# Performance work log

Hardware: AMD Instinct MI355X
Metric: run time of the kernel (lower is better)

Reference implementation:

```python
import jax, jax.numpy as jnp
from jax import lax
import numpy as np

R = 3                 # corr_radius (args.small)
NUM_LEVELS = 4        # corr_levels
SCALES = (8, 8, 4, 4, 2, 2)


def conv2d(x, w, b, pad):
    y = lax.conv_general_dilated(x, w, (1, 1), [(pad, pad), (pad, pad)],
                                 dimension_numbers=('NCHW', 'OIHW', 'NCHW'))
    return y + b[None, :, None, None]


def avg_pool2(x):
    return lax.reduce_window(x, 0.0, lax.add, (1, 1, 2, 2), (1, 1, 2, 2), 'VALID') * 0.25


def coords_grid(b, h, w):
    y, x = jnp.meshgrid(jnp.arange(h, dtype=jnp.float32), jnp.arange(w, dtype=jnp.float32), indexing='ij')
    return jnp.broadcast_to(jnp.stack([x, y])[None], (b, 2, h, w))


def bilinear_sample(img, coords):
    # img [N,C,H,W]; coords [N,Hg,Wg,2] (x,y) pixel coords; zeros padding, align_corners=True
    N, C, H, W = img.shape
    Hg, Wg = coords.shape[1], coords.shape[2]
    x, y = coords[..., 0], coords[..., 1]
    x0 = jnp.floor(x)
    y0 = jnp.floor(y)
    wx = x - x0
    wy = y - y0
    flat = img.reshape(N, C, H * W)

    def gather(xi, yi):
        valid = (xi >= 0) & (xi <= W - 1) & (yi >= 0) & (yi <= H - 1)
        xi_c = jnp.clip(xi, 0, W - 1).astype(jnp.int32)
        yi_c = jnp.clip(yi, 0, H - 1).astype(jnp.int32)
        idx = (yi_c * W + xi_c).reshape(N, 1, Hg * Wg)
        v = jnp.take_along_axis(flat, jnp.broadcast_to(idx, (N, C, Hg * Wg)), axis=2)
        return v * valid.reshape(N, 1, Hg * Wg)

    w00 = ((1 - wx) * (1 - wy)).reshape(N, 1, -1)
    w10 = (wx * (1 - wy)).reshape(N, 1, -1)
    w01 = ((1 - wx) * wy).reshape(N, 1, -1)
    w11 = (wx * wy).reshape(N, 1, -1)
    out = (gather(x0, y0) * w00 + gather(x0 + 1, y0) * w10
           + gather(x0, y0 + 1) * w01 + gather(x0 + 1, y0 + 1) * w11)
    return out.reshape(N, C, Hg, Wg)


def corr_pyramid(f1, f2):
    B, C, H, W = f1.shape
    corr = jnp.einsum('bchw,bcuv->bhwuv', f1, f2) / jnp.sqrt(jnp.float32(C))
    corr = corr.reshape(B * H * W, 1, H, W)
    pyr = [corr]
    for _ in range(NUM_LEVELS - 1):
        corr = avg_pool2(corr)
        pyr.append(corr)
    return pyr


def corr_lookup(pyr, coords):
    B, _, H, W = coords.shape
    c = coords.transpose(0, 2, 3, 1).reshape(B * H * W, 1, 1, 2)
    d = jnp.arange(-R, R + 1, dtype=jnp.float32)
    dy, dx = jnp.meshgrid(d, d, indexing='ij')
    # upstream RAFT adds stack(meshgrid(dy,dx)) to (x,y); window is symmetric so keep its ordering
    delta = jnp.stack([dy, dx], axis=-1)[None]  # [1,2R+1,2R+1,2]
    outs = []
    for i, corr in enumerate(pyr):
        cl = c / (2.0 ** i) + delta
        sampled = bilinear_sample(corr, cl)  # [B*H*W,1,2R+1,2R+1]
        outs.append(sampled.reshape(B, H, W, -1))
    return jnp.concatenate(outs, axis=-1).transpose(0, 3, 1, 2)


def interp_mat(n_in, n_out):
    # bilinear, align_corners=True
    pos = jnp.linspace(0.0, n_in - 1.0, n_out)
    i0 = jnp.clip(jnp.floor(pos).astype(jnp.int32), 0, n_in - 2)
    w = pos - i0
    M = jnp.zeros((n_out, n_in), jnp.float32)
    M = M.at[jnp.arange(n_out), i0].add(1.0 - w)
    M = M.at[jnp.arange(n_out), i0 + 1].add(w)
    return M


def upflow_n(flow, n):
    B, C, H, W = flow.shape
    My = interp_mat(H, n * H)
    Mx = interp_mat(W, n * W)
    return n * jnp.einsum('ph,bchw,qw->bcpq', My, flow, Mx)


def small_update(net, inp, corr, flow, p):
    # SmallMotionEncoder
    cor = jax.nn.relu(conv2d(corr, p['convc1_w'], p['convc1_b'], 0))
    flo = jax.nn.relu(conv2d(flow, p['convf1_w'], p['convf1_b'], 3))
    flo = jax.nn.relu(conv2d(flo, p['convf2_w'], p['convf2_b'], 1))
    mot = jax.nn.relu(conv2d(jnp.concatenate([cor, flo], 1), p['convm_w'], p['convm_b'], 1))
    x = jnp.concatenate([inp, mot, flow], 1)  # 64 + 80 + 2 = 146 ch
    # ConvGRU
    hx = jnp.concatenate([net, x], 1)
    z = jax.nn.sigmoid(conv2d(hx, p['convz_w'], p['convz_b'], 1))
    r = jax.nn.sigmoid(conv2d(hx, p['convr_w'], p['convr_b'], 1))
    q = jnp.tanh(conv2d(jnp.concatenate([r * net, x], 1), p['convq_w'], p['convq_b'], 1))
    net = (1.0 - z) * net + z * q
    # FlowHead
    df = conv2d(jax.nn.relu(conv2d(net, p['fh1_w'], p['fh1_b'], 1)), p['fh2_w'], p['fh2_b'], 1)
    return net, df


def raft_forward(fmap1_2, fmap2_2, fmap1_4, fmap2_4, fmap1_8, fmap2_8,
                 net2, inp2, net4, inp4, net8, inp8,
                 convc1_w, convc1_b, convf1_w, convf1_b, convf2_w, convf2_b,
                 convm_w, convm_b, convz_w, convz_b, convr_w, convr_b,
                 convq_w, convq_b, fh1_w, fh1_b, fh2_w, fh2_b):
    p = dict(convc1_w=convc1_w, convc1_b=convc1_b, convf1_w=convf1_w, convf1_b=convf1_b,
             convf2_w=convf2_w, convf2_b=convf2_b, convm_w=convm_w, convm_b=convm_b,
             convz_w=convz_w, convz_b=convz_b, convr_w=convr_w, convr_b=convr_b,
             convq_w=convq_w, convq_b=convq_b, fh1_w=fh1_w, fh1_b=fh1_b, fh2_w=fh2_w, fh2_b=fh2_b)
    fmaps = {2: (fmap1_2, fmap2_2), 4: (fmap1_4, fmap2_4), 8: (fmap1_8, fmap2_8)}
    pyr = {s: corr_pyramid(*fmaps[s]) for s in (2, 4, 8)}
    net = {2: jnp.tanh(net2), 4: jnp.tanh(net4), 8: jnp.tanh(net8)}
    inp = {2: jax.nn.relu(inp2), 4: jax.nn.relu(inp4), 8: jax.nn.relu(inp8)}
    B = fmap1_8.shape[0]
    coords0 = {s: coords_grid(B, fmaps[s][0].shape[2], fmaps[s][0].shape[3]) for s in (2, 4, 8)}
    coords1 = {s: coords0[s] for s in (2, 4, 8)}
    preds = []
    for s in SCALES:
        c1 = lax.stop_gradient(coords1[s])  # .detach()
        corr = corr_lookup(pyr[s], c1)
        flow = c1 - coords0[s]
        net[s], df = small_update(net[s], inp[s], corr, flow, p)
        coords1[s] = c1 + df
        preds.append(upflow_n(coords1[s] - coords0[s], s))
        if s > 2:
            coords1[s // 2] = upflow_n(coords1[s], 2)
    return jnp.stack(preds)  # [6, B, 2, 192, 192]


def setup_inputs():
    key = jax.random.key(0)
    specs = {
        'fmap1_2': (1, 128, 96, 96), 'fmap2_2': (1, 128, 96, 96),
        'fmap1_4': (1, 128, 48, 48), 'fmap2_4': (1, 128, 48, 48),
        'fmap1_8': (1, 128, 24, 24), 'fmap2_8': (1, 128, 24, 24),
        'net2': (1, 96, 96, 96), 'inp2': (1, 64, 96, 96),
        'net4': (1, 96, 48, 48), 'inp4': (1, 64, 48, 48),
        'net8': (1, 96, 24, 24), 'inp8': (1, 64, 24, 24),
        'convc1_w': (96, 196, 1, 1), 'convc1_b': (96,),
        'convf1_w': (64, 2, 7, 7), 'convf1_b': (64,),
        'convf2_w': (32, 64, 3, 3), 'convf2_b': (32,),
        'convm_w': (80, 128, 3, 3), 'convm_b': (80,),
        'convz_w': (96, 242, 3, 3), 'convz_b': (96,),
        'convr_w': (96, 242, 3, 3), 'convr_b': (96,),
        'convq_w': (96, 242, 3, 3), 'convq_b': (96,),
        'fh1_w': (128, 96, 3, 3), 'fh1_b': (128,),
        'fh2_w': (2, 128, 3, 3), 'fh2_b': (2,),
    }
    out = {}
    for i, (name, shp) in enumerate(specs.items()):
        scale = 0.1 if ('_w' in name or '_b' in name) else 1.0
        out[name] = jax.random.normal(jax.random.fold_in(key, i), shp, dtype=jnp.float32) * scale
    return out


def reference(fmap1_2, fmap2_2, fmap1_4, fmap2_4, fmap1_8, fmap2_8,
              net2, inp2, net4, inp4, net8, inp8,
              convc1_w, convc1_b, convf1_w, convf1_b, convf2_w, convf2_b,
              convm_w, convm_b, convz_w, convz_b, convr_w, convr_b,
              convq_w, convq_b, fh1_w, fh1_b, fh2_w, fh2_b):
    return raft_forward(fmap1_2, fmap2_2, fmap1_4, fmap2_4, fmap1_8, fmap2_8,
                        net2, inp2, net4, inp4, net8, inp8,
                        convc1_w, convc1_b, convf1_w, convf1_b, convf2_w, convf2_b,
                        convm_w, convm_b, convz_w, convz_b, convr_w, convr_b,
                        convq_w, convq_b, fh1_w, fh1_b, fh2_w, fh2_b)
```

## Files before the change

### kernel.cpp

```cpp
#include <hip/hip_runtime.h>
#include <hip/hip_bf16.h>
#include <math.h>


typedef __attribute__((ext_vector_type(8))) short short8;
typedef __attribute__((ext_vector_type(4))) float f32x4;

static inline int nblk(int n, int b){ return (n + b - 1) / b; }

__device__ __forceinline__ short bf16bits(float v){
  __hip_bfloat16 h = __float2bfloat16(v);
  return *reinterpret_cast<short*>(&h);
}
__device__ __forceinline__ float bf2f(short s){
  unsigned u = ((unsigned)(unsigned short)s) << 16;
  return *reinterpret_cast<float*>(&u);
}
__device__ __forceinline__ void split1(float v, unsigned short* hi, unsigned short* lo){
  short h = bf16bits(v);
  *hi = (unsigned short)h;
  *lo = (unsigned short)bf16bits(v - bf2f(h));
}
__device__ __forceinline__ int xcd_swz(int bid, int n){
  int q = n >> 3, r = n & 7;
  int x = bid & 7, k = bid >> 3;
  return (x < r ? x*(q+1) : r*(q+1) + (x-r)*q) + k;
}

__global__ void k_init_scale(const float* __restrict__ net_in, const float* __restrict__ inp_in,
                             float* __restrict__ netP, unsigned short* __restrict__ netS,
                             unsigned short* __restrict__ hxS,
                             float* __restrict__ coords, int H, int W)
{
  int HW = H*W;
  int i = blockIdx.x*256 + threadIdx.x;
  if (i >= HW*176) return;
  int p = i / 176, c = i - p*176;
  if (c < 96){
    float t = tanhf(net_in[(size_t)c*HW + p]);
    netP[(size_t)p*96 + c] = t;
    split1(t, &netS[(size_t)p*192 + c], &netS[(size_t)p*192 + 96 + c]);
  } else if (c < 160){
    float r = fmaxf(inp_in[(size_t)(c-96)*HW + p], 0.f);
    split1(r, &hxS[(size_t)p*512 + c], &hxS[(size_t)p*512 + 256 + c]);
  } else if (c < 174){
    int col = 242 + (c - 160);
    hxS[(size_t)p*512 + col] = 0;
    hxS[(size_t)p*512 + 256 + col] = 0;
  } else if (c == 174){
    coords[p] = (float)(p % W);
  } else {
    coords[HW + p] = (float)(p / W);
  }
}
__global__ void k_transpose2(const float* __restrict__ f2, const float* __restrict__ f1,
                             float* __restrict__ f2c, float* __restrict__ f1h, int HW)
{
  int i = blockIdx.x*256 + threadIdx.x;
  int n = HW*128;
  if (i >= 2*n) return;
  if (i < n){
    int p = i >> 7, c = i & 127;
    f2c[((size_t)(c >> 2)*HW + p)*4 + (c & 3)] = f2[c*HW + p];
  } else {
    int k = i - n; int p = k >> 7, c = k & 127;
    f1h[k] = f1[c*HW + p];
  }
}
__global__ void k_pool_c4(const float* __restrict__ in, float* __restrict__ out, int H2, int W2){
  int i = blockIdx.x*256 + threadIdx.x;
  int HW2 = H2*W2;
  int n = 32*HW2*4;
  if (i >= n) return;
  int e = i & 3, rest = i >> 2;
  int p = rest % HW2, cc = rest / HW2;
  int ox = p % W2, oy = p / W2;
  int Win = 2*W2;
  size_t HWin = (size_t)(2*H2)*Win;
  const float* b = in + (cc*HWin + (size_t)(2*oy)*Win + 2*ox)*4 + e;
  out[i] = 0.25f*(b[0] + b[4] + b[(size_t)Win*4] + b[(size_t)Win*4 + 4]);
}
__global__ void k_cat2(const float* __restrict__ a, const float* __restrict__ b,
                       float* __restrict__ o, int n){
  int i = blockIdx.x*256 + threadIdx.x;
  if (i < 2*n) o[i] = (i < n) ? a[i] : b[i-n];
}

__global__ __launch_bounds__(256)
void k_corr4(const float* __restrict__ f1h,
             const float* __restrict__ l0, const float* __restrict__ l1,
             const float* __restrict__ l2, const float* __restrict__ l3,
             const float* __restrict__ coords,
             unsigned short* __restrict__ corrS,
             unsigned short* __restrict__ hxS,
             const unsigned short* __restrict__ netS,
             int H, int W)
{
  int HW = H*W;
  int wv = threadIdx.x >> 6, lane = threadIdx.x & 63;
  int q = blockIdx.x*4 + wv;
  __shared__ __align__(16) float sf1[4][128];
  sf1[wv][lane]      = f1h[(size_t)q*128 + lane];
  sf1[wv][64 + lane] = f1h[(size_t)q*128 + 64 + lane];
  __syncthreads();
  float x = coords[q], y = coords[HW + q];
  const float* const lv[4] = {l0, l1, l2, l3};
  int u = lane & 7, v = lane >> 3;
  int t = lane;
  int j = min(t / 7, 6), k = min(t % 7, 6);
  const float4* a = (const float4*)&sf1[wv][0];
  #pragma unroll
  for (int i = 0; i < 4; i++){
    int Wi = W >> i, Hi = H >> i;
    size_t HWi = (size_t)Wi*Hi;
    float sc = 1.0f / (float)(1 << i);
    float xs = x*sc, ys = y*sc;
    float fx = floorf(xs), fy = floorf(ys);
    float wx = xs - fx, wy = ys - fy;
    float xf = fx + (float)(u - 3);
    float yf = fy + (float)(v - 3);
    float d = 0.0f;
    if (xf >= 0.0f && xf <= (float)(Wi-1) && yf >= 0.0f && yf <= (float)(Hi-1)){
      const float4* b = (const float4*)lv[i] + ((size_t)((int)yf)*Wi + (int)xf);
      float a0 = 0.f, a1 = 0.f, a2 = 0.f, a3 = 0.f;
      #pragma unroll
      for (int kk = 0; kk < 32; kk += 4){
        float4 av0 = a[kk],   bv0 = b[(size_t)kk*HWi];
        float4 av1 = a[kk+1], bv1 = b[(size_t)(kk+1)*HWi];
        float4 av2 = a[kk+2], bv2 = b[(size_t)(kk+2)*HWi];
        float4 av3 = a[kk+3], bv3 = b[(size_t)(kk+3)*HWi];
        a0 = fmaf(av0.x,bv0.x, fmaf(av0.y,bv0.y, fmaf(av0.z,bv0.z, fmaf(av0.w,bv0.w, a0))));
        a1 = fmaf(av1.x,bv1.x, fmaf(av1.y,bv1.y, fmaf(av1.z,bv1.z, fmaf(av1.w,bv1.w, a1))));
        a2 = fmaf(av2.x,bv2.x, fmaf(av2.y,bv2.y, fmaf(av2.z,bv2.z, fmaf(av2.w,bv2.w, a2))));
        a3 = fmaf(av3.x,bv3.x, fmaf(av3.y,bv3.y, fmaf(av3.z,bv3.z, fmaf(av3.w,bv3.w, a3))));
      }
      d = (a0 + a1) + (a2 + a3);
    }
    float d00 = __shfl(d,  k   *8 + j);
    float d10 = __shfl(d,  k   *8 + j + 1);
    float d01 = __shfl(d, (k+1)*8 + j);
    float d11 = __shfl(d, (k+1)*8 + j + 1);
    if (t < 49){
      float val = ((1.f-wx)*(1.f-wy)*d00 + wx*(1.f-wy)*d10
                + (1.f-wx)*wy*d01 + wx*wy*d11) * 0.08838834764831845f;
      split1(val, &corrS[(size_t)q*448 + i*49 + t], &corrS[(size_t)q*448 + 224 + i*49 + t]);
    }
  }
  if (lane < 28){
    corrS[(size_t)q*448 + 196 + lane] = 0;
    corrS[(size_t)q*448 + 224 + 196 + lane] = 0;
  }
  hxS[(size_t)q*512 + lane]       = netS[(size_t)q*192 + lane];
  hxS[(size_t)q*512 + 256 + lane] = netS[(size_t)q*192 + 96 + lane];
  if (lane < 32){
    hxS[(size_t)q*512 + 64 + lane]       = netS[(size_t)q*192 + 64 + lane];
    hxS[(size_t)q*512 + 256 + 64 + lane] = netS[(size_t)q*192 + 96 + 64 + lane];
  } else if (lane == 32){
    split1(x - (float)(q % W), &hxS[(size_t)q*512 + 240], &hxS[(size_t)q*512 + 256 + 240]);
  } else if (lane == 33){
    split1(y - (float)(q / W), &hxS[(size_t)q*512 + 241], &hxS[(size_t)q*512 + 256 + 241]);
  }
}

__global__ void k_upflow2(const float* __restrict__ cin, float* __restrict__ pred,
                          int Hin, int Win, float s,
                          float* __restrict__ conext, int Hf)
{
  int idx = blockIdx.x*256 + threadIdx.x;
  const int HWp = 192*192;
  int c, py, px, Hout, Wout;
  float n; int subtract; float* outp; size_t oidx;
  if (idx < 2*HWp){
    c = idx / HWp; int rem = idx - c*HWp; py = rem / 192; px = rem % 192;
    Hout = 192; Wout = 192; n = s; subtract = 1; outp = pred; oidx = idx;
  } else {
    int k2 = idx - 2*HWp;
    int HWf = Hf*Hf;
    if (Hf == 0 || k2 >= 2*HWf) return;
    c = k2 / HWf; int rem = k2 - c*HWf; py = rem / Hf; px = rem % Hf;
    Hout = Hf; Wout = Hf; n = 2.f; subtract = 0; outp = conext; oidx = k2;
  }
  float posy = (float)py * (float)(Hin-1) / (float)(Hout-1);
  float posx = (float)px * (float)(Win-1) / (float)(Wout-1);
  int iy = (int)floorf(posy); iy = max(0, min(iy, Hin-2));
  int ix = (int)floorf(posx); ix = max(0, min(ix, Win-2));
  float wy = posy - (float)iy, wx = posx - (float)ix;
  const float* base = cin + (size_t)c*Hin*Win;
  float s00 = 0.f, s10 = 0.f, s01 = 0.f, s11 = 0.f;
  if (subtract){
    if (c == 0){ s00 = (float)ix; s01 = (float)ix; s10 = (float)(ix+1); s11 = (float)(ix+1); }
    else       { s00 = (float)iy; s10 = (float)iy; s01 = (float)(iy+1); s11 = (float)(iy+1); }
  }
  float v00 = base[(size_t)iy*Win + ix]       - s00;
  float v10 = base[(size_t)iy*Win + ix + 1]   - s10;
  float v01 = base[(size_t)(iy+1)*Win + ix]   - s01;
  float v11 = base[(size_t)(iy+1)*Win + ix+1] - s11;
  float val = (1.f-wy)*((1.f-wx)*v00 + wx*v10) + wy*((1.f-wx)*v01 + wx*v11);
  outp[oidx] = n * val;
}

__global__ void k_packb(const float* __restrict__ w0, const float* __restrict__ w1,
                        int split, int Cout, int Cin, int KT, int CH32, int mode,
                        short8* __restrict__ out, int nt16, int KTN)
{
  int gid = blockIdx.x*256 + threadIdx.x;
  if (gid >= KTN*nt16*64) return;
  int lane = gid & 63, blk = gid >> 6;
  int ct = blk % nt16, kt = blk / nt16;
  int col = ct*16 + (lane & 15);
  int tap = kt / CH32, chunk = kt - tap*CH32;
  int ci0 = chunk*32 + (lane >> 4)*8;
  short8 hi8, lo8;
  #pragma unroll
  for (int e = 0; e < 8; e++){
    int ci = ci0 + e;
    float v = 0.f;
    if (col < Cout && ci < Cin && tap < KT){
      if (mode == 1){
        v = w0[((size_t)col*2 + (ci & 1))*49 + (ci >> 1)];
      } else {
        const float* wp = (col < split) ? (w0 + (size_t)col*Cin*KT)
                                        : (w1 + (size_t)(col - split)*Cin*KT);
        v = wp[(size_t)ci*KT + tap];
      }
    }
    short h = bf16bits(v);
    hi8[e] = h;
    lo8[e] = bf16bits(v - bf2f(h));
  }
  out[(size_t)blk*128 + lane]      = hi8;
  out[(size_t)blk*128 + 64 + lane] = lo8;
}

template<int KTW, int CH32, int FM, int ACT, int EPI, int NQ, int NF>
__global__ __launch_bounds__(256)
void k_fgemm(const unsigned short* __restrict__ A, int Cpad,
             const float* __restrict__ zr_, const float* __restrict__ net_,
             const float* __restrict__ coF,
             const short8* __restrict__ B, int nt16, const float* __restrict__ bias,
             float* __restrict__ outF, int osF, int ooF,
             unsigned short* __restrict__ outS, int CpadS, int ooS,
             int Cout, int H, int W,
             const float* __restrict__ ez, int ezs,
             const float* __restrict__ eold, int eos)
{
  constexpr int KT = KTW*KTW, P = KTW/2;
  int HW = H*W;
  int lane = threadIdx.x & 63;
  int nb = gridDim.x*gridDim.y;
  int wg = xcd_swz(blockIdx.y*gridDim.x + blockIdx.x, nb);
  int by = wg % gridDim.y;
  int bx = wg / gridDim.y;
  int mt = bx*4 + (threadIdx.x >> 6);
  int ct0 = by*NF;
  int p = mt*16 + (lane & 15);
  int x = p % W, y = p / W;
  int kq = (lane >> 4)*8;

  f32x4 acc[NF];
  #pragma unroll
  for (int f = 0; f < NF; f++) acc[f] = f32x4{0.f,0.f,0.f,0.f};
  const short8 zero8 = short8{0,0,0,0,0,0,0,0};

  #pragma unroll
  for (int tap = 0; tap < KT; tap++){
    const int dx = tap % KTW - P, dy = tap / KTW - P;
    int xx = x + dx, yy = y + dy;
    bool ok = ((unsigned)xx < (unsigned)W) && ((unsigned)yy < (unsigned)H);
    int base = yy*W + xx;
    const unsigned short* arow = A + (size_t)base*2*Cpad;
    #pragma unroll
    for (int c = 0; c < CH32; c++){
      int kt = tap*CH32 + c;
      short8 ah = zero8, al = zero8;
      if constexpr (FM == 2){
        float vv[8];
        #pragma unroll
        for (int e = 0; e < 8; e++){
          int ci = c*32 + kq + e;
          float v = 0.f;
          if (ci < 98){
            int t7 = ci >> 1, jj = ci & 1;
            int ddx = t7 % 7 - 3, ddy = t7 / 7 - 3;
            int x2 = x + ddx, y2 = y + ddy;
            if ((unsigned)x2 < (unsigned)W && (unsigned)y2 < (unsigned)H)
              v = coF[(size_t)jj*HW + y2*W + x2] - (float)(jj ? y2 : x2);
          }
          vv[e] = v;
        }
        #pragma unroll
        for (int e = 0; e < 8; e++){
          short h = bf16bits(vv[e]);
          ah[e] = h;
          al[e] = bf16bits(vv[e] - bf2f(h));
        }
      } else if (NQ > 0 && c < NQ){
        if (ok){
          const float4* zp = (const float4*)(zr_ + (size_t)base*192 + 96 + c*32 + kq);
          const float4* np = (const float4*)(net_ + (size_t)base*96 + c*32 + kq);
          float4 z0 = zp[0], z1 = zp[1], n0 = np[0], n1 = np[1];
          float vv[8] = {z0.x*n0.x, z0.y*n0.y, z0.z*n0.z, z0.w*n0.w,
                         z1.x*n1.x, z1.y*n1.y, z1.z*n1.z, z1.w*n1.w};
          #pragma unroll
          for (int e = 0; e < 8; e++){
            short h = bf16bits(vv[e]);
            ah[e] = h;
            al[e] = bf16bits(vv[e] - bf2f(h));
          }
        }
      } else {
        if (ok){
          const unsigned short* ap = arow + c*32 + kq;
          ah = *(const short8*)ap;
          al = *(const short8*)(ap + Cpad);
        }
      }
      const short8* bp = B + ((size_t)kt*nt16 + ct0)*128 + lane;
      #pragma unroll
      for (int f = 0; f < NF; f++){
        short8 bh = bp[(size_t)f*128], bl = bp[(size_t)f*128 + 64];
        acc[f] = __builtin_amdgcn_mfma_f32_16x16x32_bf16(ah, bh, acc[f], 0, 0, 0);
        acc[f] = __builtin_amdgcn_mfma_f32_16x16x32_bf16(al, bh, acc[f], 0, 0, 0);
        acc[f] = __builtin_amdgcn_mfma_f32_16x16x32_bf16(ah, bl, acc[f], 0, 0, 0);
      }
    }
  }

  int rowb = mt*16 + ((lane >> 4) << 2);
  int colq = lane & 15;
  #pragma unroll
  for (int f = 0; f < NF; f++){
    int col = (ct0 + f)*16 + colq;
    if (col < Cout){
      float bb = bias[col];
      #pragma unroll
      for (int r = 0; r < 4; r++){
        float val = acc[f][r] + bb;
        if (ACT == 1) val = fmaxf(val, 0.f);
        if (ACT == 2) val = 1.f/(1.f + expf(-val));
        if (ACT == 3) val = tanhf(val);
        int row = rowb + r;
        if constexpr (EPI == 2){
          outF[(size_t)col*HW + row] += val;
        } else {
          if constexpr (EPI == 1){
            float zz = ez[(size_t)row*ezs + col];
            val = (1.f - zz)*eold[(size_t)row*eos + col] + zz*val;
          }
          if constexpr (EPI == 1 || EPI == 3)
            outF[(size_t)row*osF + ooF + col] = val;
          if constexpr (EPI == 0 || EPI == 1)
            split1(val, &outS[(size_t)row*2*CpadS + ooS + col],
                        &outS[(size_t)row*2*CpadS + CpadS + ooS + col]);
        }
      }
    }
  }
}

extern "C" void kernel_launch(void* const* d_in, const int* in_sizes, int n_in,
                              void* d_out, int out_size, void* d_ws, size_t ws_size,
                              hipStream_t stream)
{
  (void)in_sizes; (void)n_in; (void)out_size; (void)ws_size;
  const float* f1s[3]    = {(const float*)d_in[0], (const float*)d_in[2], (const float*)d_in[4]};
  const float* f2s[3]    = {(const float*)d_in[1], (const float*)d_in[3], (const float*)d_in[5]};
  const float* net_in[3] = {(const float*)d_in[6], (const float*)d_in[8], (const float*)d_in[10]};
  const float* inp_in[3] = {(const float*)d_in[7], (const float*)d_in[9], (const float*)d_in[11]};
  const float* Wc1 = (const float*)d_in[12]; const float* bc1 = (const float*)d_in[13];
  const float* Wf1 = (const float*)d_in[14]; const float* bf1 = (const float*)d_in[15];
  const float* Wf2 = (const float*)d_in[16]; const float* bf2 = (const float*)d_in[17];
  const float* Wm  = (const float*)d_in[18]; const float* bm  = (const float*)d_in[19];
  const float* Wz  = (const float*)d_in[20]; const float* bz  = (const float*)d_in[21];
  const float* Wr  = (const float*)d_in[22]; const float* br  = (const float*)d_in[23];
  const float* Wq  = (const float*)d_in[24]; const float* bq  = (const float*)d_in[25];
  const float* Wh1 = (const float*)d_in[26]; const float* bh1 = (const float*)d_in[27];
  const float* Wh2 = (const float*)d_in[28]; const float* bh2 = (const float*)d_in[29];

  const int Hs[3] = {96, 48, 24};

  float* ws = (float*)d_ws;
  size_t off = 0;
  auto alloc = [&](size_t nfl)->float*{
    float* p = ws + off;
    off += (nfl + 3) & ~((size_t)3);
    return p;
  };

  float* f2l[3][4]; float* f1h[3]; float* netP[3][2]; float* coords[3];
  unsigned short* netS[3][2]; unsigned short* hxS[3];
  for (int si = 0; si < 3; si++){
    int H = Hs[si], HW = H*H;
    for (int l = 0; l < 4; l++) f2l[si][l] = alloc((size_t)(HW >> (2*l))*128);
    f1h[si]     = alloc((size_t)HW*128);
    netP[si][0] = alloc((size_t)HW*96);
    netP[si][1] = alloc((size_t)HW*96);
    netS[si][0] = (unsigned short*)alloc((size_t)HW*96);
    netS[si][1] = (unsigned short*)alloc((size_t)HW*96);
    hxS[si]     = (unsigned short*)alloc((size_t)HW*256);
    coords[si]  = alloc((size_t)2*HW);
  }
  const int HWm = 96*96;
  unsigned short* corrS = (unsigned short*)alloc((size_t)HWm*224);
  unsigned short* flo1S = (unsigned short*)alloc((size_t)HWm*64);
  unsigned short* cminS = (unsigned short*)alloc((size_t)HWm*128);
  unsigned short* t128S = (unsigned short*)alloc((size_t)HWm*128);
  float* zrb = alloc((size_t)HWm*192);
  float* Bc1 = alloc((size_t)7*6*512);
  float* Bf1 = alloc((size_t)4*4*512);
  float* Bf2 = alloc((size_t)18*2*512);
  float* Bm  = alloc((size_t)36*6*512);
  float* Bzr = alloc((size_t)72*12*512);
  float* Bq  = alloc((size_t)72*6*512);
  float* Bh1 = alloc((size_t)27*8*512);
  float* Bh2 = alloc((size_t)36*1*512);
  float* bzr = alloc(192);

  #define NB(n) dim3((unsigned)nblk((n), 256))

  k_packb<<<NB(7*6*64),  256,0,stream>>>(Wc1, Wc1, 96, 96, 196, 1, 7, 0, (short8*)Bc1, 6, 7);
  k_packb<<<NB(4*4*64),  256,0,stream>>>(Wf1, Wf1, 64, 64,  98, 1, 4, 1, (short8*)Bf1, 4, 4);
  k_packb<<<NB(18*2*64), 256,0,stream>>>(Wf2, Wf2, 32, 32,  64, 9, 2, 0, (short8*)Bf2, 2, 18);
  k_packb<<<NB(36*6*64), 256,0,stream>>>(Wm,  Wm,  80, 80, 128, 9, 4, 0, (short8*)Bm,  6, 36);
  k_packb<<<NB(72*12*64),256,0,stream>>>(Wz,  Wr,  96, 192,242, 9, 8, 0, (short8*)Bzr, 12, 72);
  k_packb<<<NB(72*6*64), 256,0,stream>>>(Wq,  Wq,  96, 96, 242, 9, 8, 0, (short8*)Bq,  6, 72);
  k_packb<<<NB(27*8*64), 256,0,stream>>>(Wh1, Wh1,128, 128, 96, 9, 3, 0, (short8*)Bh1, 8, 27);
  k_packb<<<NB(36*1*64), 256,0,stream>>>(Wh2, Wh2,  2,   2,128, 9, 4, 0, (short8*)Bh2, 1, 36);
  k_cat2<<<dim3(1), 256, 0, stream>>>(bz, br, bzr, 96);

  for (int si = 0; si < 3; si++){
    int H = Hs[si], HW = H*H;
    k_init_scale<<<NB(HW*176), 256,0,stream>>>(net_in[si], inp_in[si], netP[si][0],
                                               netS[si][0], hxS[si], coords[si], H, H);
    k_transpose2<<<NB(2*HW*128), 256,0,stream>>>(f2s[si], f1s[si], f2l[si][0], f1h[si], HW);
    for (int l = 1; l < 4; l++){
      int Hl = H >> l;
      k_pool_c4<<<NB(32*Hl*Hl*4), 256,0,stream>>>(f2l[si][l-1], f2l[si][l], Hl, Hl);
    }
  }

  int cur[3] = {0, 0, 0};
  const int seq[6] = {2, 2, 1, 1, 0, 0};
  for (int it = 0; it < 6; it++){
    int si = seq[it];
    int H = Hs[si], W = H, HW = H*W;
    int MT = HW/16;
    float s = (si == 0) ? 2.0f : ((si == 1) ? 4.0f : 8.0f);
    float* netcF = netP[si][cur[si]];
    float* netnF = netP[si][cur[si]^1];
    unsigned short* netcS = netS[si][cur[si]];
    unsigned short* netnS = netS[si][cur[si]^1];
    float* co = coords[si];
    unsigned short* hx = hxS[si];
    unsigned gx = (unsigned)(MT/4);

    k_corr4<<<dim3((unsigned)(HW/4)), 256,0,stream>>>(
        f1h[si], f2l[si][0], f2l[si][1], f2l[si][2], f2l[si][3], co,
        corrS, hx, netcS, H, W);

    k_fgemm<1,7,0,1,0,0,2><<<dim3(gx,3), 256,0,stream>>>(corrS,224, nullptr,nullptr,nullptr,
        (short8*)Bc1, 6, bc1, nullptr,0,0, cminS,128,0, 96, H,W, nullptr,0, nullptr,0);
    k_fgemm<1,4,2,1,0,0,2><<<dim3(gx,2), 256,0,stream>>>(nullptr,0, nullptr,nullptr,co,
        (short8*)Bf1, 4, bf1, nullptr,0,0, flo1S,64,0, 64, H,W, nullptr,0, nullptr,0);
    k_fgemm<3,2,0,1,0,0,2><<<dim3(gx,1), 256,0,stream>>>(flo1S,64, nullptr,nullptr,nullptr,
        (short8*)Bf2, 2, bf2, nullptr,0,0, cminS,128,96, 32, H,W, nullptr,0, nullptr,0);
    k_fgemm<3,4,0,1,0,0,2><<<dim3(gx,3), 256,0,stream>>>(cminS,128, nullptr,nullptr,nullptr,
        (short8*)Bm, 6, bm, nullptr,0,0, hx,256,160, 80, H,W, nullptr,0, nullptr,0);
    k_fgemm<3,8,0,2,3,0,2><<<dim3(gx,6), 256,0,stream>>>(hx,256, nullptr,nullptr,nullptr,
        (short8*)Bzr, 12, bzr, zrb,192,0, nullptr,0,0, 192, H,W, nullptr,0, nullptr,0);
    k_fgemm<3,8,0,3,1,3,2><<<dim3(gx,3), 256,0,stream>>>(hx,256, zrb,netcF,nullptr,
        (short8*)Bq, 6, bq, netnF,96,0, netnS,96,0, 96, H,W, zrb,192, netcF,96);
    k_fgemm<3,3,0,1,0,0,2><<<dim3(gx,4), 256,0,stream>>>(netnS,96, nullptr,nullptr,nullptr,
        (short8*)Bh1, 8, bh1, nullptr,0,0, t128S,128,0, 128, H,W, nullptr,0, nullptr,0);
    k_fgemm<3,4,0,0,2,0,1><<<dim3(gx,1), 256,0,stream>>>(t128S,128, nullptr,nullptr,nullptr,
        (short8*)Bh2, 1, bh2, co,0,0, nullptr,0,0, 2, H,W, nullptr,0, nullptr,0);

    int Hf = (si > 0) ? Hs[si-1] : 0;
    float* conext = (si > 0) ? coords[si-1] : nullptr;
    k_upflow2<<<NB(2*192*192 + (Hf ? 2*Hf*Hf : 0)), 256,0,stream>>>(
        co, (float*)d_out + (size_t)it*2*192*192, H, W, s, conext, Hf);

    cur[si] ^= 1;
  }
  #undef NB
}
```

Measured before the change: 1.335 ms.

## Store bf16 activations in zero-padded halo layout and widen N-tiles for largest scale

Intermediate split-bf16 activation buffers (net, hx, flow, corr-motion, hidden) are now allocated per scale with a one-pixel zero border and memset once, so the 3x3 conv GEMM loads no longer need bounds checks or predicated zero fills. Epilogues write into the padded coordinates. For the largest scale, the GEMMs also use more output fragments per wave (NF 3 or 4) with fewer column blocks, trading more registers for better B-operand reuse and fewer A reloads. Costs are extra memory, a memset, and per-scale buffer copies instead of shared ones.

Result: slower. 1.454 ms (+8.9%).

```diff
diff --git a/kernel.cpp b/kernel.cpp
--- a/kernel.cpp
+++ b/kernel.cpp
@@ -34,20 +34,18 @@
 {
   int HW = H*W;
   int i = blockIdx.x*256 + threadIdx.x;
-  if (i >= HW*176) return;
-  int p = i / 176, c = i - p*176;
+  if (i >= HW*162) return;
+  int p = i / 162, c = i - p*162;
+  int PW = W + 2;
+  size_t pq = (size_t)(p / W + 1)*PW + (p % W) + 1;
   if (c < 96){
     float t = tanhf(net_in[(size_t)c*HW + p]);
     netP[(size_t)p*96 + c] = t;
-    split1(t, &netS[(size_t)p*192 + c], &netS[(size_t)p*192 + 96 + c]);
+    split1(t, &netS[pq*192 + c], &netS[pq*192 + 96 + c]);
   } else if (c < 160){
     float r = fmaxf(inp_in[(size_t)(c-96)*HW + p], 0.f);
-    split1(r, &hxS[(size_t)p*512 + c], &hxS[(size_t)p*512 + 256 + c]);
-  } else if (c < 174){
-    int col = 242 + (c - 160);
-    hxS[(size_t)p*512 + col] = 0;
-    hxS[(size_t)p*512 + 256 + col] = 0;
-  } else if (c == 174){
+    split1(r, &hxS[pq*512 + c], &hxS[pq*512 + 256 + c]);
+  } else if (c == 160){
     coords[p] = (float)(p % W);
   } else {
     coords[HW + p] = (float)(p / W);
@@ -150,15 +148,17 @@
     corrS[(size_t)q*448 + 196 + lane] = 0;
     corrS[(size_t)q*448 + 224 + 196 + lane] = 0;
   }
-  hxS[(size_t)q*512 + lane]       = netS[(size_t)q*192 + lane];
-  hxS[(size_t)q*512 + 256 + lane] = netS[(size_t)q*192 + 96 + lane];
+  int PW = W + 2;
+  size_t pq = (size_t)(q / W + 1)*PW + (q % W) + 1;
+  hxS[pq*512 + lane]       = netS[pq*192 + lane];
+  hxS[pq*512 + 256 + lane] = netS[pq*192 + 96 + lane];
   if (lane < 32){
-    hxS[(size_t)q*512 + 64 + lane]       = netS[(size_t)q*192 + 64 + lane];
-    hxS[(size_t)q*512 + 256 + 64 + lane] = netS[(size_t)q*192 + 96 + 64 + lane];
+    hxS[pq*512 + 64 + lane]       = netS[pq*192 + 64 + lane];
+    hxS[pq*512 + 256 + 64 + lane] = netS[pq*192 + 96 + 64 + lane];
   } else if (lane == 32){
-    split1(x - (float)(q % W), &hxS[(size_t)q*512 + 240], &hxS[(size_t)q*512 + 256 + 240]);
+    split1(x - (float)(q % W), &hxS[pq*512 + 240], &hxS[pq*512 + 256 + 240]);
   } else if (lane == 33){
-    split1(y - (float)(q / W), &hxS[(size_t)q*512 + 241], &hxS[(size_t)q*512 + 256 + 241]);
+    split1(y - (float)(q / W), &hxS[pq*512 + 241], &hxS[pq*512 + 256 + 241]);
   }
 }
 
@@ -232,7 +232,7 @@
   out[(size_t)blk*128 + 64 + lane] = lo8;
 }
 
-template<int KTW, int CH32, int FM, int ACT, int EPI, int NQ, int NF>
+template<int KTW, int CH32, int FM, int ACT, int EPI, int NQ, int NF, int PAD>
 __global__ __launch_bounds__(256)
 void k_fgemm(const unsigned short* __restrict__ A, int Cpad,
              const float* __restrict__ zr_, const float* __restrict__ net_,
@@ -246,6 +246,7 @@
 {
   constexpr int KT = KTW*KTW, P = KTW/2;
   int HW = H*W;
+  int PW = W + 2;
   int lane = threadIdx.x & 63;
   int nb = gridDim.x*gridDim.y;
   int wg = xcd_swz(blockIdx.y*gridDim.x + blockIdx.x, nb);
@@ -266,9 +267,17 @@
   for (int tap = 0; tap < KT; tap++){
     const int dx = tap % KTW - P, dy = tap / KTW - P;
     int xx = x + dx, yy = y + dy;
-    bool ok = ((unsigned)xx < (unsigned)W) && ((unsigned)yy < (unsigned)H);
-    int base = yy*W + xx;
-    const unsigned short* arow = A + (size_t)base*2*Cpad;
+    const unsigned short* arow;
+    bool ok;
+    if (PAD){
+      arow = A + (size_t)((yy+1)*PW + xx + 1)*2*Cpad;
+      ok = true;
+    } else {
+      ok = ((unsigned)xx < (unsigned)W) && ((unsigned)yy < (unsigned)H);
+      arow = A + (size_t)(yy*W + xx)*2*Cpad;
+    }
+    int baseu = yy*W + xx;
+    bool okq = ((unsigned)xx < (unsigned)W) && ((unsigned)yy < (unsigned)H);
     #pragma unroll
     for (int c = 0; c < CH32; c++){
       int kt = tap*CH32 + c;
@@ -295,9 +304,9 @@
           al[e] = bf16bits(vv[e] - bf2f(h));
         }
       } else if (NQ > 0 && c < NQ){
-        if (ok){
-          const float4* zp = (const float4*)(zr_ + (size_t)base*192 + 96 + c*32 + kq);
-          const float4* np = (const float4*)(net_ + (size_t)base*96 + c*32 + kq);
+        if (okq){
+          const float4* zp = (const float4*)(zr_ + (size_t)baseu*192 + 96 + c*32 + kq);
+          const float4* np = (const float4*)(net_ + (size_t)baseu*96 + c*32 + kq);
           float4 z0 = zp[0], z1 = zp[1], n0 = np[0], n1 = np[1];
           float vv[8] = {z0.x*n0.x, z0.y*n0.y, z0.z*n0.z, z0.w*n0.w,
                          z1.x*n1.x, z1.y*n1.y, z1.z*n1.z, z1.w*n1.w};
@@ -309,7 +318,7 @@
           }
         }
       } else {
-        if (ok){
+        if (PAD || ok){
           const unsigned short* ap = arow + c*32 + kq;
           ah = *(const short8*)ap;
           al = *(const short8*)(ap + Cpad);
@@ -349,9 +358,12 @@
           }
           if constexpr (EPI == 1 || EPI == 3)
             outF[(size_t)row*osF + ooF + col] = val;
-          if constexpr (EPI == 0 || EPI == 1)
-            split1(val, &outS[(size_t)row*2*CpadS + ooS + col],
-                        &outS[(size_t)row*2*CpadS + CpadS + ooS + col]);
+          if constexpr (EPI == 0 || EPI == 1){
+            int pyo = row / W, pxo = row - pyo*W;
+            size_t op = (size_t)((pyo+1)*PW + pxo + 1);
+            split1(val, &outS[op*2*CpadS + ooS + col],
+                        &outS[op*2*CpadS + CpadS + ooS + col]);
+          }
         }
       }
     }
@@ -388,23 +400,16 @@
   };
 
   float* f2l[3][4]; float* f1h[3]; float* netP[3][2]; float* coords[3];
-  unsigned short* netS[3][2]; unsigned short* hxS[3];
   for (int si = 0; si < 3; si++){
     int H = Hs[si], HW = H*H;
     for (int l = 0; l < 4; l++) f2l[si][l] = alloc((size_t)(HW >> (2*l))*128);
     f1h[si]     = alloc((size_t)HW*128);
     netP[si][0] = alloc((size_t)HW*96);
     netP[si][1] = alloc((size_t)HW*96);
-    netS[si][0] = (unsigned short*)alloc((size_t)HW*96);
-    netS[si][1] = (unsigned short*)alloc((size_t)HW*96);
-    hxS[si]     = (unsigned short*)alloc((size_t)HW*256);
     coords[si]  = alloc((size_t)2*HW);
   }
   const int HWm = 96*96;
   unsigned short* corrS = (unsigned short*)alloc((size_t)HWm*224);
-  unsigned short* flo1S = (unsigned short*)alloc((size_t)HWm*64);
-  unsigned short* cminS = (unsigned short*)alloc((size_t)HWm*128);
-  unsigned short* t128S = (unsigned short*)alloc((size_t)HWm*128);
   float* zrb = alloc((size_t)HWm*192);
   float* Bc1 = alloc((size_t)7*6*512);
   float* Bf1 = alloc((size_t)4*4*512);
@@ -416,6 +421,22 @@
   float* Bh2 = alloc((size_t)36*1*512);
   float* bzr = alloc(192);
 
+  float* padBase = ws + off;
+  unsigned short* netS[3][2]; unsigned short* hxS[3];
+  unsigned short* flo1S[3]; unsigned short* cminS[3]; unsigned short* t128S[3];
+  for (int si = 0; si < 3; si++){
+    int PH = Hs[si] + 2;
+    size_t PP = (size_t)PH*PH;
+    netS[si][0] = (unsigned short*)alloc(PP*96);
+    netS[si][1] = (unsigned short*)alloc(PP*96);
+    hxS[si]     = (unsigned short*)alloc(PP*256);
+    flo1S[si]   = (unsigned short*)alloc(PP*64);
+    cminS[si]   = (unsigned short*)alloc(PP*128);
+    t128S[si]   = (unsigned short*)alloc(PP*128);
+  }
+  size_t padBytes = (size_t)((ws + off) - padBase) * 4;
+  hipMemsetAsync(padBase, 0, padBytes, stream);
+
   #define NB(n) dim3((unsigned)nblk((n), 256))
 
   k_packb<<<NB(7*6*64),  256,0,stream>>>(Wc1, Wc1, 96, 96, 196, 1, 7, 0, (short8*)Bc1, 6, 7);
@@ -430,7 +451,7 @@
 
   for (int si = 0; si < 3; si++){
     int H = Hs[si], HW = H*H;
-    k_init_scale<<<NB(HW*176), 256,0,stream>>>(net_in[si], inp_in[si], netP[si][0],
+    k_init_scale<<<NB(HW*162), 256,0,stream>>>(net_in[si], inp_in[si], netP[si][0],
                                                netS[si][0], hxS[si], coords[si], H, H);
     k_transpose2<<<NB(2*HW*128), 256,0,stream>>>(f2s[si], f1s[si], f2l[si][0], f1h[si], HW);
     for (int l = 1; l < 4; l++){
@@ -453,26 +474,37 @@
     float* co = coords[si];
     unsigned short* hx = hxS[si];
     unsigned gx = (unsigned)(MT/4);
+    bool big = (si == 0);
 
     k_corr4<<<dim3((unsigned)(HW/4)), 256,0,stream>>>(
         f1h[si], f2l[si][0], f2l[si][1], f2l[si][2], f2l[si][3], co,
         corrS, hx, netcS, H, W);
 
-    k_fgemm<1,7,0,1,0,0,2><<<dim3(gx,3), 256,0,stream>>>(corrS,224, nullptr,nullptr,nullptr,
-        (short8*)Bc1, 6, bc1, nullptr,0,0, cminS,128,0, 96, H,W, nullptr,0, nullptr,0);
-    k_fgemm<1,4,2,1,0,0,2><<<dim3(gx,2), 256,0,stream>>>(nullptr,0, nullptr,nullptr,co,
-        (short8*)Bf1, 4, bf1, nullptr,0,0, flo1S,64,0, 64, H,W, nullptr,0, nullptr,0);
-    k_fgemm<3,2,0,1,0,0,2><<<dim3(gx,1), 256,0,stream>>>(flo1S,64, nullptr,nullptr,nullptr,
-        (short8*)Bf2, 2, bf2, nullptr,0,0, cminS,128,96, 32, H,W, nullptr,0, nullptr,0);
-    k_fgemm<3,4,0,1,0,0,2><<<dim3(gx,3), 256,0,stream>>>(cminS,128, nullptr,nullptr,nullptr,
+    if (big) k_fgemm<1,7,0,1,0,0,3,0><<<dim3(gx,2), 256,0,stream>>>(corrS,224, nullptr,nullptr,nullptr,
+        (short8*)Bc1, 6, bc1, nullptr,0,0, cminS[si],128,0, 96, H,W, nullptr,0, nullptr,0);
+    else     k_fgemm<1,7,0,1,0,0,2,0><<<dim3(gx,3), 256,0,stream>>>(corrS,224, nullptr,nullptr,nullptr,
+        (short8*)Bc1, 6, bc1, nullptr,0,0, cminS[si],128,0, 96, H,W, nullptr,0, nullptr,0);
+    k_fgemm<1,4,2,1,0,0,2,0><<<dim3(gx,2), 256,0,stream>>>(nullptr,0, nullptr,nullptr,co,
+        (short8*)Bf1, 4, bf1, nullptr,0,0, flo1S[si],64,0, 64, H,W, nullptr,0, nullptr,0);
+    k_fgemm<3,2,0,1,0,0,2,1><<<dim3(gx,1), 256,0,stream>>>(flo1S[si],64, nullptr,nullptr,nullptr,
+        (short8*)Bf2, 2, bf2, nullptr,0,0, cminS[si],128,96, 32, H,W, nullptr,0, nullptr,0);
+    if (big) k_fgemm<3,4,0,1,0,0,3,1><<<dim3(gx,2), 256,0,stream>>>(cminS[si],128, nullptr,nullptr,nullptr,
         (short8*)Bm, 6, bm, nullptr,0,0, hx,256,160, 80, H,W, nullptr,0, nullptr,0);
-    k_fgemm<3,8,0,2,3,0,2><<<dim3(gx,6), 256,0,stream>>>(hx,256, nullptr,nullptr,nullptr,
+    else     k_fgemm<3,4,0,1,0,0,2,1><<<dim3(gx,3), 256,0,stream>>>(cminS[si],128, nullptr,nullptr,nullptr,
+        (short8*)Bm, 6, bm, nullptr,0,0, hx,256,160, 80, H,W, nullptr,0, nullptr,0);
+    if (big) k_fgemm<3,8,0,2,3,0,4,1><<<dim3(gx,3), 256,0,stream>>>(hx,256, nullptr,nullptr,nullptr,
         (short8*)Bzr, 12, bzr, zrb,192,0, nullptr,0,0, 192, H,W, nullptr,0, nullptr,0);
-    k_fgemm<3,8,0,3,1,3,2><<<dim3(gx,3), 256,0,stream>>>(hx,256, zrb,netcF,nullptr,
+    else     k_fgemm<3,8,0,2,3,0,2,1><<<dim3(gx,6), 256,0,stream>>>(hx,256, nullptr,nullptr,nullptr,
+        (short8*)Bzr, 12, bzr, zrb,192,0, nullptr,0,0, 192, H,W, nullptr,0, nullptr,0);
+    if (big) k_fgemm<3,8,0,3,1,3,3,1><<<dim3(gx,2), 256,0,stream>>>(hx,256, zrb,netcF,nullptr,
         (short8*)Bq, 6, bq, netnF,96,0, netnS,96,0, 96, H,W, zrb,192, netcF,96);
-    k_fgemm<3,3,0,1,0,0,2><<<dim3(gx,4), 256,0,stream>>>(netnS,96, nullptr,nullptr,nullptr,
-        (short8*)Bh1, 8, bh1, nullptr,0,0, t128S,128,0, 128, H,W, nullptr,0, nullptr,0);
-    k_fgemm<3,4,0,0,2,0,1><<<dim3(gx,1), 256,0,stream>>>(t128S,128, nullptr,nullptr,nullptr,
+    else     k_fgemm<3,8,0,3,1,3,2,1><<<dim3(gx,3), 256,0,stream>>>(hx,256, zrb,netcF,nullptr,
+        (short8*)Bq, 6, bq, netnF,96,0, netnS,96,0, 96, H,W, zrb,192, netcF,96);
+    if (big) k_fgemm<3,3,0,1,0,0,4,1><<<dim3(gx,2), 256,0,stream>>>(netnS,96, nullptr,nullptr,nullptr,
+        (short8*)Bh1, 8, bh1, nullptr,0,0, t128S[si],128,0, 128, H,W, nullptr,0, nullptr,0);
+    else     k_fgemm<3,3,0,1,0,0,2,1><<<dim3(gx,4), 256,0,stream>>>(netnS,96, nullptr,nullptr,nullptr,
+        (short8*)Bh1, 8, bh1, nullptr,0,0, t128S[si],128,0, 128, H,W, nullptr,0, nullptr,0);
+    k_fgemm<3,4,0,0,2,0,1,1><<<dim3(gx,1), 256,0,stream>>>(t128S[si],128, nullptr,nullptr,nullptr,
         (short8*)Bh2, 1, bh2, co,0,0, nullptr,0,0, 2, H,W, nullptr,0, nullptr,0);
 
     int Hf = (si > 0) ? Hs[si-1] : 0;
```

## Split-K over taps with partial-sum reduction and wider N tiles at largest scale

Applied to the files above, without the earlier changes.

At the largest scale (96x96), the z/r, q and first flow-head convolutions split their 3x3 taps across two grid slices. Each slice writes raw partial accumulators, and a new elementwise reduce kernel adds the slices, applies bias and activation, and does the GRU or bf16-split epilogue. The corr and motion convs at that scale also take more column tiles per workgroup (NF 3 instead of 2), so each A fragment is reused across more tiles and fewer blocks are launched. The change trades extra partial-sum memory traffic and added kernel launches for less A reloading and shorter per-block K loops.

Result: faster. 1.283 ms (-3.9%).

```diff
diff --git a/kernel.cpp b/kernel.cpp
--- a/kernel.cpp
+++ b/kernel.cpp
@@ -232,7 +232,32 @@
   out[(size_t)blk*128 + 64 + lane] = lo8;
 }
 
-template<int KTW, int CH32, int FM, int ACT, int EPI, int NQ, int NF>
+template<int ACT, int MODE>
+__global__ void k_red(const float* __restrict__ part, int NP, int HW,
+                      const float* __restrict__ bias,
+                      float* __restrict__ outF, unsigned short* __restrict__ outS,
+                      const float* __restrict__ ez, const float* __restrict__ eold)
+{
+  int i = blockIdx.x*256 + threadIdx.x;
+  if (i >= HW*NP) return;
+  int row = i / NP, col = i - row*NP;
+  float val = part[i] + part[(size_t)HW*NP + i] + bias[col];
+  if (ACT == 1) val = fmaxf(val, 0.f);
+  if (ACT == 2) val = 1.f/(1.f + expf(-val));
+  if (ACT == 3) val = tanhf(val);
+  if constexpr (MODE == 0){
+    outF[i] = val;
+  } else if constexpr (MODE == 1){
+    float zz = ez[(size_t)row*192 + col];
+    val = (1.f - zz)*eold[(size_t)row*96 + col] + zz*val;
+    outF[(size_t)row*96 + col] = val;
+    split1(val, &outS[(size_t)row*192 + col], &outS[(size_t)row*192 + 96 + col]);
+  } else {
+    split1(val, &outS[(size_t)row*2*NP + col], &outS[(size_t)row*2*NP + NP + col]);
+  }
+}
+
+template<int KTW, int CH32, int FM, int ACT, int EPI, int NQ, int NF, int KS>
 __global__ __launch_bounds__(256)
 void k_fgemm(const unsigned short* __restrict__ A, int Cpad,
              const float* __restrict__ zr_, const float* __restrict__ net_,
@@ -245,8 +270,10 @@
              const float* __restrict__ eold, int eos)
 {
   constexpr int KT = KTW*KTW, P = KTW/2;
+  constexpr int TPZ = (KS > 1) ? (KT + KS - 1)/KS : KT;
   int HW = H*W;
   int lane = threadIdx.x & 63;
+  int kz = (KS > 1) ? (int)blockIdx.z : 0;
   int nb = gridDim.x*gridDim.y;
   int wg = xcd_swz(blockIdx.y*gridDim.x + blockIdx.x, nb);
   int by = wg % gridDim.y;
@@ -263,8 +290,10 @@
   const short8 zero8 = short8{0,0,0,0,0,0,0,0};
 
   #pragma unroll
-  for (int tap = 0; tap < KT; tap++){
-    const int dx = tap % KTW - P, dy = tap / KTW - P;
+  for (int tt = 0; tt < TPZ; tt++){
+    int tap = kz*TPZ + tt;
+    if (KS > 1 && tap >= KT) break;
+    int dx = tap % KTW - P, dy = tap / KTW - P;
     int xx = x + dx, yy = y + dy;
     bool ok = ((unsigned)xx < (unsigned)W) && ((unsigned)yy < (unsigned)H);
     int base = yy*W + xx;
@@ -328,6 +357,7 @@
 
   int rowb = mt*16 + ((lane >> 4) << 2);
   int colq = lane & 15;
+  size_t pOff = (KS > 1) ? (size_t)kz*HW*osF : 0;
   #pragma unroll
   for (int f = 0; f < NF; f++){
     int col = (ct0 + f)*16 + colq;
@@ -335,23 +365,27 @@
       float bb = bias[col];
       #pragma unroll
       for (int r = 0; r < 4; r++){
-        float val = acc[f][r] + bb;
-        if (ACT == 1) val = fmaxf(val, 0.f);
-        if (ACT == 2) val = 1.f/(1.f + expf(-val));
-        if (ACT == 3) val = tanhf(val);
         int row = rowb + r;
-        if constexpr (EPI == 2){
-          outF[(size_t)col*HW + row] += val;
+        if constexpr (EPI == 4){
+          outF[pOff + (size_t)row*osF + ooF + col] = acc[f][r];
         } else {
-          if constexpr (EPI == 1){
-            float zz = ez[(size_t)row*ezs + col];
-            val = (1.f - zz)*eold[(size_t)row*eos + col] + zz*val;
+          float val = acc[f][r] + bb;
+          if (ACT == 1) val = fmaxf(val, 0.f);
+          if (ACT == 2) val = 1.f/(1.f + expf(-val));
+          if (ACT == 3) val = tanhf(val);
+          if constexpr (EPI == 2){
+            outF[(size_t)col*HW + row] += val;
+          } else {
+            if constexpr (EPI == 1){
+              float zz = ez[(size_t)row*ezs + col];
+              val = (1.f - zz)*eold[(size_t)row*eos + col] + zz*val;
+            }
+            if constexpr (EPI == 1 || EPI == 3)
+              outF[(size_t)row*osF + ooF + col] = val;
+            if constexpr (EPI == 0 || EPI == 1)
+              split1(val, &outS[(size_t)row*2*CpadS + ooS + col],
+                          &outS[(size_t)row*2*CpadS + CpadS + ooS + col]);
           }
-          if constexpr (EPI == 1 || EPI == 3)
-            outF[(size_t)row*osF + ooF + col] = val;
-          if constexpr (EPI == 0 || EPI == 1)
-            split1(val, &outS[(size_t)row*2*CpadS + ooS + col],
-                        &outS[(size_t)row*2*CpadS + CpadS + ooS + col]);
         }
       }
     }
@@ -405,7 +439,8 @@
   unsigned short* flo1S = (unsigned short*)alloc((size_t)HWm*64);
   unsigned short* cminS = (unsigned short*)alloc((size_t)HWm*128);
   unsigned short* t128S = (unsigned short*)alloc((size_t)HWm*128);
-  float* zrb = alloc((size_t)HWm*192);
+  float* zrb   = alloc((size_t)HWm*192);
+  float* partP = alloc((size_t)2*HWm*192);
   float* Bc1 = alloc((size_t)7*6*512);
   float* Bf1 = alloc((size_t)4*4*512);
   float* Bf2 = alloc((size_t)18*2*512);
@@ -453,26 +488,49 @@
     float* co = coords[si];
     unsigned short* hx = hxS[si];
     unsigned gx = (unsigned)(MT/4);
+    bool big = (si == 0);
 
     k_corr4<<<dim3((unsigned)(HW/4)), 256,0,stream>>>(
         f1h[si], f2l[si][0], f2l[si][1], f2l[si][2], f2l[si][3], co,
         corrS, hx, netcS, H, W);
 
-    k_fgemm<1,7,0,1,0,0,2><<<dim3(gx,3), 256,0,stream>>>(corrS,224, nullptr,nullptr,nullptr,
+    if (big) k_fgemm<1,7,0,1,0,0,3,1><<<dim3(gx,2), 256,0,stream>>>(corrS,224, nullptr,nullptr,nullptr,
         (short8*)Bc1, 6, bc1, nullptr,0,0, cminS,128,0, 96, H,W, nullptr,0, nullptr,0);
-    k_fgemm<1,4,2,1,0,0,2><<<dim3(gx,2), 256,0,stream>>>(nullptr,0, nullptr,nullptr,co,
+    else     k_fgemm<1,7,0,1,0,0,2,1><<<dim3(gx,3), 256,0,stream>>>(corrS,224, nullptr,nullptr,nullptr,
+        (short8*)Bc1, 6, bc1, nullptr,0,0, cminS,128,0, 96, H,W, nullptr,0, nullptr,0);
+    k_fgemm<1,4,2,1,0,0,2,1><<<dim3(gx,2), 256,0,stream>>>(nullptr,0, nullptr,nullptr,co,
         (short8*)Bf1, 4, bf1, nullptr,0,0, flo1S,64,0, 64, H,W, nullptr,0, nullptr,0);
-    k_fgemm<3,2,0,1,0,0,2><<<dim3(gx,1), 256,0,stream>>>(flo1S,64, nullptr,nullptr,nullptr,
+    k_fgemm<3,2,0,1,0,0,2,1><<<dim3(gx,1), 256,0,stream>>>(flo1S,64, nullptr,nullptr,nullptr,
         (short8*)Bf2, 2, bf2, nullptr,0,0, cminS,128,96, 32, H,W, nullptr,0, nullptr,0);
-    k_fgemm<3,4,0,1,0,0,2><<<dim3(gx,3), 256,0,stream>>>(cminS,128, nullptr,nullptr,nullptr,
+    if (big) k_fgemm<3,4,0,1,0,0,3,1><<<dim3(gx,2), 256,0,stream>>>(cminS,128, nullptr,nullptr,nullptr,
         (short8*)Bm, 6, bm, nullptr,0,0, hx,256,160, 80, H,W, nullptr,0, nullptr,0);
-    k_fgemm<3,8,0,2,3,0,2><<<dim3(gx,6), 256,0,stream>>>(hx,256, nullptr,nullptr,nullptr,
-        (short8*)Bzr, 12, bzr, zrb,192,0, nullptr,0,0, 192, H,W, nullptr,0, nullptr,0);
-    k_fgemm<3,8,0,3,1,3,2><<<dim3(gx,3), 256,0,stream>>>(hx,256, zrb,netcF,nullptr,
-        (short8*)Bq, 6, bq, netnF,96,0, netnS,96,0, 96, H,W, zrb,192, netcF,96);
-    k_fgemm<3,3,0,1,0,0,2><<<dim3(gx,4), 256,0,stream>>>(netnS,96, nullptr,nullptr,nullptr,
-        (short8*)Bh1, 8, bh1, nullptr,0,0, t128S,128,0, 128, H,W, nullptr,0, nullptr,0);
-    k_fgemm<3,4,0,0,2,0,1><<<dim3(gx,1), 256,0,stream>>>(t128S,128, nullptr,nullptr,nullptr,
+    else     k_fgemm<3,4,0,1,0,0,2,1><<<dim3(gx,3), 256,0,stream>>>(cminS,128, nullptr,nullptr,nullptr,
+        (short8*)Bm, 6, bm, nullptr,0,0, hx,256,160, 80, H,W, nullptr,0, nullptr,0);
+    if (big){
+      k_fgemm<3,8,0,0,4,0,4,2><<<dim3(gx,3,2), 256,0,stream>>>(hx,256, nullptr,nullptr,nullptr,
+          (short8*)Bzr, 12, bzr, partP,192,0, nullptr,0,0, 192, H,W, nullptr,0, nullptr,0);
+      k_red<2,0><<<NB(HW*192), 256,0,stream>>>(partP, 192, HW, bzr, zrb, nullptr, nullptr, nullptr);
+    } else {
+      k_fgemm<3,8,0,2,3,0,2,1><<<dim3(gx,6), 256,0,stream>>>(hx,256, nullptr,nullptr,nullptr,
+          (short8*)Bzr, 12, bzr, zrb,192,0, nullptr,0,0, 192, H,W, nullptr,0, nullptr,0);
+    }
+    if (big){
+      k_fgemm<3,8,0,0,4,3,3,2><<<dim3(gx,2,2), 256,0,stream>>>(hx,256, zrb,netcF,nullptr,
+          (short8*)Bq, 6, bq, partP,96,0, nullptr,0,0, 96, H,W, nullptr,0, nullptr,0);
+      k_red<3,1><<<NB(HW*96), 256,0,stream>>>(partP, 96, HW, bq, netnF, netnS, zrb, netcF);
+    } else {
+      k_fgemm<3,8,0,3,1,3,2,1><<<dim3(gx,3), 256,0,stream>>>(hx,256, zrb,netcF,nullptr,
+          (short8*)Bq, 6, bq, netnF,96,0, netnS,96,0, 96, H,W, zrb,192, netcF,96);
+    }
+    if (big){
+      k_fgemm<3,3,0,0,4,0,4,2><<<dim3(gx,2,2), 256,0,stream>>>(netnS,96, nullptr,nullptr,nullptr,
+          (short8*)Bh1, 8, bh1, partP,128,0, nullptr,0,0, 128, H,W, nullptr,0, nullptr,0);
+      k_red<1,2><<<NB(HW*128), 256,0,stream>>>(partP, 128, HW, bh1, nullptr, t128S, nullptr, nullptr);
+    } else {
+      k_fgemm<3,3,0,1,0,0,2,1><<<dim3(gx,4), 256,0,stream>>>(netnS,96, nullptr,nullptr,nullptr,
+          (short8*)Bh1, 8, bh1, nullptr,0,0, t128S,128,0, 128, H,W, nullptr,0, nullptr,0);
+    }
+    k_fgemm<3,4,0,0,2,0,1,1><<<dim3(gx,1), 256,0,stream>>>(t128S,128, nullptr,nullptr,nullptr,
         (short8*)Bh2, 1, bh2, co,0,0, nullptr,0,0, 2, H,W, nullptr,0, nullptr,0);
 
     int Hf = (si > 0) ? Hs[si-1] : 0;
```
